# Performance work log

Hardware: AMD Instinct MI355X
Metric: run time of the kernel (lower is better)

Reference implementation:

```python
import jax, jax.numpy as jnp
import numpy as np

EPS = 1e-5  # torch InstanceNorm3d default eps


def setup_inputs() -> dict:
    key = jax.random.key(0)
    kx, kw, kb = jax.random.split(key, 3)
    # x: (B, C_in, T, D, H, W)
    x = jax.random.normal(kx, (1, 4, 8, 96, 96, 96), dtype=jnp.float32)
    # 4D hypercube conv kernel: (C_out, C_in, kT, kD, kH, kW)
    w = jax.random.normal(kw, (8, 4, 3, 3, 3, 3), dtype=jnp.float32) * 0.05
    b = jax.random.normal(kb, (8,), dtype=jnp.float32) * 0.05
    return {"x": x, "w": w, "b": b}


def reference(x, w, b):
    # Per-time-slice InstanceNorm3d (affine=False): normalizing each t-slice
    # over (D,H,W) per (b,c) is identical to normalizing over spatial dims
    # per (b,c,t) in one fused pass (the torch loop + stack is just this).
    mean = jnp.mean(x, axis=(3, 4, 5), keepdims=True)
    var = jnp.var(x, axis=(3, 4, 5), keepdims=True)  # biased, as in torch
    xn = (x - mean) * jax.lax.rsqrt(var + EPS)
    # ReLU activation
    xa = jax.nn.relu(xn)
    # True 4D convolution (T,D,H,W spatial), padding=1 everywhere, stride 1.
    # This equals the repo's Conv4d (sum of per-temporal-offset Conv3d's).
    out = jax.lax.conv_general_dilated(
        xa, w,
        window_strides=(1, 1, 1, 1),
        padding=[(1, 1)] * 4,
        dimension_numbers=("NCTDHW", "OITDHW", "NCTDHW"),
    )
    return out + b.reshape(1, -1, 1, 1, 1, 1)
```

## Files before the change

### kernel.cpp

```cpp
#include <hip/hip_runtime.h>

#define CI 4
#define CO 8
#define TT 8
#define S 96
#define SLICE (S*S*S)
#define NSLICE (CI*TT)
#define EPS 1e-5f
#define WTOT (CO*CI*81)
#define WS_WT_OFF 64


__global__ __launch_bounds__(256) void stats_partial(
        const float* __restrict__ x, float* __restrict__ ws) {
    const int slice = blockIdx.y;
    const float4* p = reinterpret_cast<const float4*>(x + (size_t)slice * SLICE);
    const int n4 = SLICE / 4;
    float s = 0.f, ss = 0.f;
    for (int i = blockIdx.x * blockDim.x + threadIdx.x; i < n4;
         i += gridDim.x * blockDim.x) {
        float4 v = p[i];
        s  += v.x + v.y + v.z + v.w;
        ss += v.x*v.x + v.y*v.y + v.z*v.z + v.w*v.w;
    }
    #pragma unroll
    for (int off = 32; off > 0; off >>= 1) {
        s  += __shfl_down(s, off);
        ss += __shfl_down(ss, off);
    }
    __shared__ float ls[4], lss[4];
    const int lane = threadIdx.x & 63, wid = threadIdx.x >> 6;
    if (lane == 0) { ls[wid] = s; lss[wid] = ss; }
    __syncthreads();
    if (threadIdx.x == 0) {
        float ts  = ls[0] + ls[1] + ls[2] + ls[3];
        float tss = lss[0] + lss[1] + lss[2] + lss[3];
        atomicAdd(&ws[slice], ts);
        atomicAdd(&ws[NSLICE + slice], tss);
    }
}

__global__ void wtranspose(const float* __restrict__ w, float* __restrict__ wt) {
    int i = blockIdx.x * blockDim.x + threadIdx.x;
    if (i >= WTOT) return;
    int kw = i % 3; int r = i / 3;
    int co = r % CO; r /= CO;
    int kh = r % 3;  r /= 3;
    int kd = r % 3;  r /= 3;
    int kt = r % 3;  r /= 3;
    int ci = r;
    wt[i] = w[((((co * CI + ci) * 3 + kt) * 3 + kd) * 3 + kh) * 3 + kw];
}

__device__ __forceinline__ void load_rows(
        const float* __restrict__ xp, int h0, int w0, int om1, int op4,
        float4 f4[4], float e0[4], float e1[4]) {
    #pragma unroll
    for (int r = 0; r < 4; r++) {
        const int hh = h0 + r - 1;
        const int hc = hh < 0 ? 0 : (hh > S - 1 ? S - 1 : hh);
        const float* row = xp + hc * S + w0;
        f4[r] = *reinterpret_cast<const float4*>(row);
        e0[r] = row[om1];
        e1[r] = row[op4];
    }
}

template <bool TW>
__device__ __forceinline__ void compute_kd(
        const float4 f4[4], const float e0[4], const float e1[4],
        float rstd, float nmr, float md, int h0, float fwl, float fwr,
        const float* __restrict__ wp, float acc[2][CO][4]) {
    float n[4][6];
    #pragma unroll
    for (int r = 0; r < 4; r++) {
        const int hh = h0 + r - 1;
        const float m_ = (((unsigned)hh < S) ? 1.f : 0.f) * md;
        const float rs = rstd * m_, nm = nmr * m_;
        n[r][0] = fwl * fmaxf(fmaf(e0[r],   rs, nm), 0.f);
        n[r][1] =       fmaxf(fmaf(f4[r].x, rs, nm), 0.f);
        n[r][2] =       fmaxf(fmaf(f4[r].y, rs, nm), 0.f);
        n[r][3] =       fmaxf(fmaf(f4[r].z, rs, nm), 0.f);
        n[r][4] =       fmaxf(fmaf(f4[r].w, rs, nm), 0.f);
        n[r][5] = fwr * fmaxf(fmaf(e1[r],   rs, nm), 0.f);
    }
    #pragma unroll
    for (int kh = 0; kh < 3; kh++) {
        #pragma unroll
        for (int co = 0; co < CO; co++) {
            const float* wc = TW ? (wp + kh * 24 + co * 3)
                                 : (wp + co * (CI * 81) + kh * 3);
            const float k0 = wc[0], k1 = wc[1], k2 = wc[2];
            #pragma unroll
            for (int j = 0; j < 4; j++) {
                float a0 = acc[0][co][j];
                a0 = fmaf(n[kh][j],     k0, a0);
                a0 = fmaf(n[kh][j + 1], k1, a0);
                a0 = fmaf(n[kh][j + 2], k2, a0);
                acc[0][co][j] = a0;
                float a1 = acc[1][co][j];
                a1 = fmaf(n[kh + 1][j],     k0, a1);
                a1 = fmaf(n[kh + 1][j + 1], k1, a1);
                a1 = fmaf(n[kh + 1][j + 2], k2, a1);
                acc[1][co][j] = a1;
            }
        }
    }
}

template <bool TW>
__global__ __launch_bounds__(192, 3) void conv4d_fused(
        const float* __restrict__ x, const float* __restrict__ wsrc,
        const float* __restrict__ bias, const float* __restrict__ ws,
        float* __restrict__ out) {
    const int lane = threadIdx.x;
    const int ty   = threadIdx.y;
    const int w0   = lane << 2;
    const int d    = blockIdx.x;
    const int h0   = (blockIdx.y * 8 + ty) * 2;
    const int t    = blockIdx.z;

    float acc[2][CO][4];
    #pragma unroll
    for (int p = 0; p < 2; p++)
        #pragma unroll
        for (int co = 0; co < CO; co++)
            #pragma unroll
            for (int j = 0; j < 4; j++) acc[p][co][j] = 0.f;

    const bool wlb = (lane > 0), wrb = (lane < 23);
    const int  om1 = wlb ? -1 : 0;
    const int  op4 = wrb ?  4 : 3;
    const float fwl = wlb ? 1.f : 0.f, fwr = wrb ? 1.f : 0.f;
    const float inv_n = 1.f / (float)SLICE;

    const int dm1 = d > 0 ? d - 1 : 0;
    const int dp1 = d < S - 1 ? d + 1 : S - 1;
    const float md0 = d > 0 ? 1.f : 0.f;
    const float md2 = d < S - 1 ? 1.f : 0.f;

    float4 fA[4], fB[4];
    float eA0[4], eA1[4], eB0[4], eB1[4];

    for (int ci = 0; ci < CI; ci++) {
        for (int kt = 0; kt < 3; kt++) {
            const int tt = t + kt - 1;
            if ((unsigned)tt >= TT) continue;
            const int sl = ci * TT + tt;
            const float mean = ws[sl] * inv_n;
            const float var  = ws[NSLICE + sl] * inv_n - mean * mean;
            const float rstd = rsqrtf(var + EPS);
            const float nmr  = -mean * rstd;
            const float* xs = x + (size_t)sl * SLICE;
            const float* xp0 = xs + (size_t)dm1 * (S * S);
            const float* xp1 = xs + (size_t)d   * (S * S);
            const float* xp2 = xs + (size_t)dp1 * (S * S);
            const float* wp = TW ? (wsrc + (ci * 3 + kt) * 216)
                                 : (wsrc + ci * 81 + kt * 27);

            load_rows(xp0, h0, w0, om1, op4, fA, eA0, eA1);
            load_rows(xp1, h0, w0, om1, op4, fB, eB0, eB1);
            compute_kd<TW>(fA, eA0, eA1, rstd, nmr, md0, h0, fwl, fwr,
                           TW ? wp : wp, acc);
            load_rows(xp2, h0, w0, om1, op4, fA, eA0, eA1);
            compute_kd<TW>(fB, eB0, eB1, rstd, nmr, 1.f, h0, fwl, fwr,
                           TW ? wp + 72 : wp + 9, acc);
            compute_kd<TW>(fA, eA0, eA1, rstd, nmr, md2, h0, fwl, fwr,
                           TW ? wp + 144 : wp + 18, acc);
        }
    }

    #pragma unroll
    for (int p = 0; p < 2; p++) {
        const size_t obase = (((size_t)t * S + d) * S + (h0 + p)) * S + w0;
        #pragma unroll
        for (int co = 0; co < CO; co++) {
            const float bb = bias[co];
            float4 o;
            o.x = acc[p][co][0] + bb;
            o.y = acc[p][co][1] + bb;
            o.z = acc[p][co][2] + bb;
            o.w = acc[p][co][3] + bb;
            *reinterpret_cast<float4*>(out + (size_t)co * ((size_t)TT * SLICE) + obase) = o;
        }
    }
}

extern "C" void kernel_launch(void* const* d_in, const int* in_sizes, int n_in,
                              void* d_out, int out_size, void* d_ws, size_t ws_size,
                              hipStream_t stream) {
    const float* x   = (const float*)d_in[0];
    const float* w   = (const float*)d_in[1];
    const float* b   = (const float*)d_in[2];
    float* out = (float*)d_out;
    float* ws  = (float*)d_ws;

    const bool tw = ws_size >= (size_t)(WS_WT_OFF + WTOT) * sizeof(float);

    hipMemsetAsync(ws, 0, 2 * NSLICE * sizeof(float), stream);
    stats_partial<<<dim3(64, NSLICE), 256, 0, stream>>>(x, ws);
    if (tw) {
        wtranspose<<<(WTOT + 255) / 256, 256, 0, stream>>>(w, ws + WS_WT_OFF);
        conv4d_fused<true><<<dim3(S, S / 16, TT), dim3(24, 8, 1), 0, stream>>>(
                x, ws + WS_WT_OFF, b, ws, out);
    } else {
        conv4d_fused<false><<<dim3(S, S / 16, TT), dim3(24, 8, 1), 0, stream>>>(
                x, w, b, ws, out);
    }
}
```

Before: 787.6 us.

## Software-pipeline row loads across ci/kt iterations with triple buffering

Restructures the conv main loop into a flattened ci×kt iteration that uses three register buffers, so loads for the next slice's d-1 and d planes are issued while the current slice's planes are being computed. Row offsets and H-boundary masks are hoisted out of the loop. The aim is to hide global-load latency behind FMA work. The extra live registers risk spills or lower occupancy under launch_bounds(192,3).

```diff
diff --git a/kernel.cpp b/kernel.cpp
--- a/kernel.cpp
+++ b/kernel.cpp
@@ -4,6 +4,7 @@
 #define CO 8
 #define TT 8
 #define S 96
+#define S2 (S*S)
 #define SLICE (S*S*S)
 #define NSLICE (CI*TT)
 #define EPS 1e-5f
@@ -52,62 +53,6 @@
     wt[i] = w[((((co * CI + ci) * 3 + kt) * 3 + kd) * 3 + kh) * 3 + kw];
 }
 
-__device__ __forceinline__ void load_rows(
-        const float* __restrict__ xp, int h0, int w0, int om1, int op4,
-        float4 f4[4], float e0[4], float e1[4]) {
-    #pragma unroll
-    for (int r = 0; r < 4; r++) {
-        const int hh = h0 + r - 1;
-        const int hc = hh < 0 ? 0 : (hh > S - 1 ? S - 1 : hh);
-        const float* row = xp + hc * S + w0;
-        f4[r] = *reinterpret_cast<const float4*>(row);
-        e0[r] = row[om1];
-        e1[r] = row[op4];
-    }
-}
-
-template <bool TW>
-__device__ __forceinline__ void compute_kd(
-        const float4 f4[4], const float e0[4], const float e1[4],
-        float rstd, float nmr, float md, int h0, float fwl, float fwr,
-        const float* __restrict__ wp, float acc[2][CO][4]) {
-    float n[4][6];
-    #pragma unroll
-    for (int r = 0; r < 4; r++) {
-        const int hh = h0 + r - 1;
-        const float m_ = (((unsigned)hh < S) ? 1.f : 0.f) * md;
-        const float rs = rstd * m_, nm = nmr * m_;
-        n[r][0] = fwl * fmaxf(fmaf(e0[r],   rs, nm), 0.f);
-        n[r][1] =       fmaxf(fmaf(f4[r].x, rs, nm), 0.f);
-        n[r][2] =       fmaxf(fmaf(f4[r].y, rs, nm), 0.f);
-        n[r][3] =       fmaxf(fmaf(f4[r].z, rs, nm), 0.f);
-        n[r][4] =       fmaxf(fmaf(f4[r].w, rs, nm), 0.f);
-        n[r][5] = fwr * fmaxf(fmaf(e1[r],   rs, nm), 0.f);
-    }
-    #pragma unroll
-    for (int kh = 0; kh < 3; kh++) {
-        #pragma unroll
-        for (int co = 0; co < CO; co++) {
-            const float* wc = TW ? (wp + kh * 24 + co * 3)
-                                 : (wp + co * (CI * 81) + kh * 3);
-            const float k0 = wc[0], k1 = wc[1], k2 = wc[2];
-            #pragma unroll
-            for (int j = 0; j < 4; j++) {
-                float a0 = acc[0][co][j];
-                a0 = fmaf(n[kh][j],     k0, a0);
-                a0 = fmaf(n[kh][j + 1], k1, a0);
-                a0 = fmaf(n[kh][j + 2], k2, a0);
-                acc[0][co][j] = a0;
-                float a1 = acc[1][co][j];
-                a1 = fmaf(n[kh + 1][j],     k0, a1);
-                a1 = fmaf(n[kh + 1][j + 1], k1, a1);
-                a1 = fmaf(n[kh + 1][j + 2], k2, a1);
-                acc[1][co][j] = a1;
-            }
-        }
-    }
-}
-
 template <bool TW>
 __global__ __launch_bounds__(192, 3) void conv4d_fused(
         const float* __restrict__ x, const float* __restrict__ wsrc,
@@ -138,37 +83,136 @@
     const int dp1 = d < S - 1 ? d + 1 : S - 1;
     const float md0 = d > 0 ? 1.f : 0.f;
     const float md2 = d < S - 1 ? 1.f : 0.f;
-
-    float4 fA[4], fB[4];
-    float eA0[4], eA1[4], eB0[4], eB1[4];
-
-    for (int ci = 0; ci < CI; ci++) {
-        for (int kt = 0; kt < 3; kt++) {
-            const int tt = t + kt - 1;
-            if ((unsigned)tt >= TT) continue;
-            const int sl = ci * TT + tt;
-            const float mean = ws[sl] * inv_n;
-            const float var  = ws[NSLICE + sl] * inv_n - mean * mean;
-            const float rstd = rsqrtf(var + EPS);
-            const float nmr  = -mean * rstd;
-            const float* xs = x + (size_t)sl * SLICE;
-            const float* xp0 = xs + (size_t)dm1 * (S * S);
-            const float* xp1 = xs + (size_t)d   * (S * S);
-            const float* xp2 = xs + (size_t)dp1 * (S * S);
-            const float* wp = TW ? (wsrc + (ci * 3 + kt) * 216)
-                                 : (wsrc + ci * 81 + kt * 27);
-
-            load_rows(xp0, h0, w0, om1, op4, fA, eA0, eA1);
-            load_rows(xp1, h0, w0, om1, op4, fB, eB0, eB1);
-            compute_kd<TW>(fA, eA0, eA1, rstd, nmr, md0, h0, fwl, fwr,
-                           TW ? wp : wp, acc);
-            load_rows(xp2, h0, w0, om1, op4, fA, eA0, eA1);
-            compute_kd<TW>(fB, eB0, eB1, rstd, nmr, 1.f, h0, fwl, fwr,
-                           TW ? wp + 72 : wp + 9, acc);
-            compute_kd<TW>(fA, eA0, eA1, rstd, nmr, md2, h0, fwl, fwr,
-                           TW ? wp + 144 : wp + 18, acc);
+    int   off[4];
+    float mr0, mr1, mr2, mr3;
+    {
+        const int hh0 = h0 - 1, hh1 = h0, hh2 = h0 + 1, hh3 = h0 + 2;
+        mr0 = ((unsigned)hh0 < S) ? 1.f : 0.f;
+        mr1 = 1.f; mr2 = 1.f;
+        mr3 = ((unsigned)hh3 < S) ? 1.f : 0.f;
+        const int hc0 = hh0 < 0 ? 0 : hh0;
+        const int hc3 = hh3 > S - 1 ? S - 1 : hh3;
+        off[0] = hc0 * S + w0; off[1] = hh1 * S + w0;
+        off[2] = hh2 * S + w0; off[3] = hc3 * S + w0;
+    }
+    const int o0 = off[0], o1 = off[1], o2 = off[2], o3 = off[3];
+
+    const int ktlo = (t == 0) ? 1 : 0;
+    const int kthi = (t == TT - 1) ? 1 : 2;
+    const int nkt  = kthi - ktlo + 1;
+    const int niter = CI * nkt;
+
+    #define DECL_BUF(N) \
+        float4 f##N##0, f##N##1, f##N##2, f##N##3; \
+        float e##N##00, e##N##01, e##N##02, e##N##03; \
+        float e##N##10, e##N##11, e##N##12, e##N##13;
+    DECL_BUF(A) DECL_BUF(B) DECL_BUF(C)
+
+    #define LOAD_BUF(N, XP) do { \
+        const float* _r0 = (XP) + o0; const float* _r1 = (XP) + o1; \
+        const float* _r2 = (XP) + o2; const float* _r3 = (XP) + o3; \
+        f##N##0 = *reinterpret_cast<const float4*>(_r0); \
+        f##N##1 = *reinterpret_cast<const float4*>(_r1); \
+        f##N##2 = *reinterpret_cast<const float4*>(_r2); \
+        f##N##3 = *reinterpret_cast<const float4*>(_r3); \
+        e##N##00 = _r0[om1]; e##N##01 = _r1[om1]; \
+        e##N##02 = _r2[om1]; e##N##03 = _r3[om1]; \
+        e##N##10 = _r0[op4]; e##N##11 = _r1[op4]; \
+        e##N##12 = _r2[op4]; e##N##13 = _r3[op4]; \
+    } while (0)
+
+    #define NORM_ROW(N, R, MR, MD) do { \
+        const float m_ = (MR) * (MD); \
+        const float rs = rstd * m_, nm = nmr * m_; \
+        nn[R][0] = fwl * fmaxf(fmaf(e##N##0##R, rs, nm), 0.f); \
+        nn[R][1] =       fmaxf(fmaf(f##N##R.x,  rs, nm), 0.f); \
+        nn[R][2] =       fmaxf(fmaf(f##N##R.y,  rs, nm), 0.f); \
+        nn[R][3] =       fmaxf(fmaf(f##N##R.z,  rs, nm), 0.f); \
+        nn[R][4] =       fmaxf(fmaf(f##N##R.w,  rs, nm), 0.f); \
+        nn[R][5] = fwr * fmaxf(fmaf(e##N##1##R, rs, nm), 0.f); \
+    } while (0)
+
+    #define COMPUTE_BUF(N, WP, MD) do { \
+        float nn[4][6]; \
+        NORM_ROW(N, 0, mr0, MD); NORM_ROW(N, 1, mr1, MD); \
+        NORM_ROW(N, 2, mr2, MD); NORM_ROW(N, 3, mr3, MD); \
+        _Pragma("unroll") \
+        for (int kh = 0; kh < 3; kh++) { \
+            _Pragma("unroll") \
+            for (int co = 0; co < CO; co++) { \
+                const float* wc = TW ? ((WP) + kh * 24 + co * 3) \
+                                     : ((WP) + co * (CI * 81) + kh * 3); \
+                const float k0 = wc[0], k1 = wc[1], k2 = wc[2]; \
+                _Pragma("unroll") \
+                for (int j = 0; j < 4; j++) { \
+                    float a0 = acc[0][co][j]; \
+                    a0 = fmaf(nn[kh][j],     k0, a0); \
+                    a0 = fmaf(nn[kh][j + 1], k1, a0); \
+                    a0 = fmaf(nn[kh][j + 2], k2, a0); \
+                    acc[0][co][j] = a0; \
+                    float a1 = acc[1][co][j]; \
+                    a1 = fmaf(nn[kh + 1][j],     k0, a1); \
+                    a1 = fmaf(nn[kh + 1][j + 1], k1, a1); \
+                    a1 = fmaf(nn[kh + 1][j + 2], k2, a1); \
+                    acc[1][co][j] = a1; \
+                } \
+            } \
+        } \
+    } while (0)
+
+    int ci = 0, kt = ktlo;
+    int sl = ci * TT + (t + kt - 1);
+    const float* xs = x + (size_t)sl * SLICE;
+    const float* xp2;
+    float rstd, nmr;
+    {
+        const float mean = ws[sl] * inv_n;
+        const float var  = ws[NSLICE + sl] * inv_n - mean * mean;
+        rstd = rsqrtf(var + EPS);
+        nmr  = -mean * rstd;
+    }
+    const float* wp = TW ? (wsrc + (ci * 3 + kt) * 216)
+                         : (wsrc + ci * 81 + kt * 27);
+    xp2 = xs + (size_t)dp1 * S2;
+    LOAD_BUF(A, xs + (size_t)dm1 * S2);
+    LOAD_BUF(B, xs + (size_t)d   * S2);
+
+    for (int it = 0; it < niter; it++) {
+        LOAD_BUF(C, xp2);
+
+        COMPUTE_BUF(A, TW ? wp : wp, md0);
+
+        int kt_n = kt, ci_n = ci;
+        if (it + 1 < niter) {
+            kt_n = kt + 1;
+            if (kt_n > kthi) { kt_n = ktlo; ci_n = ci + 1; }
         }
-    }
+        const int sl_n = ci_n * TT + (t + kt_n - 1);
+        const float* xs_n = x + (size_t)sl_n * SLICE;
+        const float mean_n = ws[sl_n] * inv_n;
+        const float var_n  = ws[NSLICE + sl_n] * inv_n - mean_n * mean_n;
+        const float rstd_n = rsqrtf(var_n + EPS);
+        const float nmr_n  = -mean_n * rstd_n;
+        const float* wp_n = TW ? (wsrc + (ci_n * 3 + kt_n) * 216)
+                               : (wsrc + ci_n * 81 + kt_n * 27);
+
+        LOAD_BUF(A, xs_n + (size_t)dm1 * S2);
+
+        COMPUTE_BUF(B, TW ? wp + 72 : wp + 9, 1.f);
+
+        LOAD_BUF(B, xs_n + (size_t)d * S2);
+
+        COMPUTE_BUF(C, TW ? wp + 144 : wp + 18, md2);
+
+        rstd = rstd_n; nmr = nmr_n; wp = wp_n;
+        xp2 = xs_n + (size_t)dp1 * S2;
+        ci = ci_n; kt = kt_n;
+    }
+
+    #undef DECL_BUF
+    #undef LOAD_BUF
+    #undef NORM_ROW
+    #undef COMPUTE_BUF
 
     #pragma unroll
     for (int p = 0; p < 2; p++) {
```

Measured after the change: 656.9 us. -16.6%, faster.
